# Performance work log

Measured on AMD Instinct MI355X. Metric: run time of the kernel, lower is better.

The kernel has to match this reference:

```python
import jax, jax.numpy as jnp
import numpy as np

RES = (128, 128, 128, 100)  # x, y, z, t resolutions
FEAT = 64
N = 1048576
HID = 64
COMBOS4 = [(0, 1), (0, 2), (0, 3), (1, 2), (1, 3), (2, 3)]  # temporal k-planes
COMBOS3 = [(0, 1), (0, 2), (1, 2)]  # spatial triplane


def setup_inputs() -> dict:
    key = jax.random.key(0)
    ks = jax.random.split(key, 16)
    d = {}
    d["inp"] = jax.random.uniform(ks[0], (N, 4), dtype=jnp.float32)  # xyz in [0,1], t in [0,1]
    d["aabb"] = jnp.array([[0.0, 0.0, 0.0], [1.0, 1.0, 1.0]], dtype=jnp.float32)
    # plane coefs: [feat, res[b], res[a]] per combo (a,b), uniform(init_a, init_b)
    for i, (a, b) in enumerate(COMBOS4):
        d[f"tp{i}"] = jax.random.uniform(ks[1 + i], (FEAT, RES[b], RES[a]),
                                         minval=0.1, maxval=0.5, dtype=jnp.float32)
    for i, (a, b) in enumerate(COMBOS3):
        d[f"sp{i}"] = jax.random.uniform(ks[7 + i], (FEAT, RES[b], RES[a]),
                                         minval=0.1, maxval=0.5, dtype=jnp.float32)
    in_dim = 2 * FEAT  # temporal + spatial features concatenated
    d["w0"] = (jax.random.normal(ks[10], (in_dim, HID), dtype=jnp.float32) / np.sqrt(in_dim)).astype(jnp.float32)
    d["b0"] = jnp.zeros((HID,), dtype=jnp.float32)
    d["w1"] = (jax.random.normal(ks[11], (HID, 3), dtype=jnp.float32) / np.sqrt(HID)).astype(jnp.float32)
    d["b1"] = jnp.zeros((3,), dtype=jnp.float32)
    return d


def _sample_plane(plane, cx, cy):
    """Bilinear grid_sample, align_corners=True. plane: [F,H,W]; cx,cy: [N] in [-1,1]. Returns [N,F]."""
    F_, H, W = plane.shape
    x = (cx + 1.0) * 0.5 * (W - 1)
    y = (cy + 1.0) * 0.5 * (H - 1)
    x0 = jnp.clip(jnp.floor(x).astype(jnp.int32), 0, W - 2)
    y0 = jnp.clip(jnp.floor(y).astype(jnp.int32), 0, H - 2)
    wx = (x - x0)[:, None]
    wy = (y - y0)[:, None]
    p = jnp.transpose(plane, (1, 2, 0))  # [H,W,F]
    v00 = p[y0, x0]
    v01 = p[y0, x0 + 1]
    v10 = p[y0 + 1, x0]
    v11 = p[y0 + 1, x0 + 1]
    return (v00 * (1 - wx) + v01 * wx) * (1 - wy) + (v10 * (1 - wx) + v11 * wx) * wy


def reference(inp, aabb, tp0, tp1, tp2, tp3, tp4, tp5, sp0, sp1, sp2, w0, b0, w1, b1):
    # normalize positions to [-1,1]
    pos = (inp[:, :3] - aabb[0]) / (aabb[1] - aabb[0]) * 2.0 - 1.0
    t = inp[:, 3:] * 2.0 - 1.0
    c = jnp.concatenate([pos, t], axis=-1)  # [N,4]
    tps = [tp0, tp1, tp2, tp3, tp4, tp5]
    feat_t = sum(_sample_plane(tps[i], c[:, a], c[:, b]) for i, (a, b) in enumerate(COMBOS4))
    sps = [sp0, sp1, sp2]
    feat_s = sum(_sample_plane(sps[i], pos[:, a], pos[:, b]) for i, (a, b) in enumerate(COMBOS3))
    feat = jnp.concatenate([feat_t, feat_s], axis=-1)  # [N, 2*FEAT]
    h = jax.nn.relu(feat @ w0 + b0)
    return h @ w1 + b1  # [N, 3]
```

## Files before the change

kernel.cpp:

```cpp
#include <hip/hip_runtime.h>
#include <hip/hip_fp16.h>

#define DEVFN __device__ __forceinline__

#if defined(__has_builtin)
#  if __has_builtin(__builtin_amdgcn_fdot2)
#    define HAS_FDOT2 1
#  endif
#endif

typedef _Float16 h2v __attribute__((ext_vector_type(2)));

struct PlanePtrs { const float* p[9]; };

__constant__ const int g_H[9] = {128,128,100,128,100,100,128,128,128};
__constant__ const int g_A[9] = {0,0,0,1,1,2,0,0,1};
__constant__ const int g_B[9] = {1,2,3,2,3,3,1,2,2};
__constant__ const int g_PRE[10] = {0,16384,32768,45568,61952,74752,87552,103936,120320,136704};
__constant__ const int g_OFF4[9] = {0,131072,262144,364544,495616,598016,700416,831488,962560};

static const int    TOTAL_TEXELS = 136704;
static const size_t WS_PLANES    = 17498112ull;
static const size_t WS_W0H       = 16384ull;
static const int    NBINS        = 2048;
static const int    NHB          = 256;

__global__ __launch_bounds__(256) void k_transpose(PlanePtrs ptrs, __half* __restrict__ dst)
{
    int gid = blockIdx.x * 256 + threadIdx.x;

    int pl = 0;
    #pragma unroll
    for (int i = 1; i < 9; ++i) if (gid >= g_PRE[i]) pl = i;
    int tx   = gid - g_PRE[pl];
    int nTex = g_PRE[pl + 1] - g_PRE[pl];

    const float* src = ptrs.p[0];
    #pragma unroll
    for (int i = 1; i < 9; ++i) if (pl == i) src = ptrs.p[i];
    src += tx;

    uint4* __restrict__ out4 = reinterpret_cast<uint4*>(dst) + (size_t)gid * 8;
    #pragma unroll
    for (int j = 0; j < 8; ++j) {
        float f0 = src[(8*j+0)*nTex];
        float f1 = src[(8*j+1)*nTex];
        float f2 = src[(8*j+2)*nTex];
        float f3 = src[(8*j+3)*nTex];
        float f4 = src[(8*j+4)*nTex];
        float f5 = src[(8*j+5)*nTex];
        float f6 = src[(8*j+6)*nTex];
        float f7 = src[(8*j+7)*nTex];
        uint4 u;
        u.x = __builtin_bit_cast(unsigned int, __floats2half2_rn(f0, f1));
        u.y = __builtin_bit_cast(unsigned int, __floats2half2_rn(f2, f3));
        u.z = __builtin_bit_cast(unsigned int, __floats2half2_rn(f4, f5));
        u.w = __builtin_bit_cast(unsigned int, __floats2half2_rn(f6, f7));
        out4[j] = u;
    }
}

__global__ __launch_bounds__(256) void k_w0pack(const float* __restrict__ w0,
                                                unsigned int* __restrict__ w0h)
{
    int idx = blockIdx.x * 256 + threadIdx.x;
    int d = idx >> 6, j = idx & 63;
    float a = w0[(2 * d) * 64 + j];
    float b = w0[(2 * d + 1) * 64 + j];
    w0h[idx] = __builtin_bit_cast(unsigned int, __floats2half2_rn(a, b));
}

DEVFN int point_key(float4 in, float a0x, float a0y, float a0z,
                    float isx, float isy, float isz)
{
    float x = (in.x - a0x) * isx;
    float y = (in.y - a0y) * isy;
    float z = (in.z - a0z) * isz;
    int xc = min(7, max(0, (int)(x * 8.0f)));
    int yc = min(7, max(0, (int)(y * 8.0f)));
    int zc = min(7, max(0, (int)(z * 8.0f)));
    int tc = min(3, max(0, (int)(in.w * 4.0f)));
    return (((xc << 3) | yc) << 3 | zc) << 2 | tc;
}

__global__ __launch_bounds__(256) void k_hist2(const float4* __restrict__ inp,
                                               const float* __restrict__ aabb,
                                               int N, int chunk,
                                               int* __restrict__ blkhist)
{
    __shared__ int hc[NBINS];
    const int tid = threadIdx.x, blk = blockIdx.x;
    #pragma unroll
    for (int j = 0; j < NBINS / 256; ++j) hc[tid + j * 256] = 0;
    __syncthreads();

    float a0x = aabb[0], a0y = aabb[1], a0z = aabb[2];
    float isx = 1.0f / (aabb[3] - a0x), isy = 1.0f / (aabb[4] - a0y), isz = 1.0f / (aabb[5] - a0z);

    int end = min(N, (blk + 1) * chunk);
    for (int i = blk * chunk + tid; i < end; i += 256)
        atomicAdd(&hc[point_key(inp[i], a0x, a0y, a0z, isx, isy, isz)], 1);

    __syncthreads();
    #pragma unroll
    for (int j = 0; j < NBINS / 256; ++j)
        blkhist[blk * NBINS + tid + j * 256] = hc[tid + j * 256];
}

__global__ __launch_bounds__(256) void k_scanA(int* __restrict__ blkhist,
                                               int* __restrict__ bintotal)
{
    int bin = blockIdx.x * 256 + threadIdx.x;
    int run = 0;
    for (int b = 0; b < NHB; ++b) {
        int v = blkhist[b * NBINS + bin];
        blkhist[b * NBINS + bin] = run;
        run += v;
    }
    bintotal[bin] = run;
}

__global__ __launch_bounds__(256) void k_scanB(const int* __restrict__ bintotal,
                                               int* __restrict__ binstart)
{
    int t = threadIdx.x;
    int v[8]; int sum = 0;
    #pragma unroll
    for (int j = 0; j < 8; ++j) { v[j] = bintotal[t * 8 + j]; sum += v[j]; }

    int lane = t & 63, w = t >> 6;
    int x = sum;
    #pragma unroll
    for (int d = 1; d < 64; d <<= 1) {
        int y = __shfl_up(x, d);
        if (lane >= d) x += y;
    }
    __shared__ int wsum[4];
    if (lane == 63) wsum[w] = x;
    __syncthreads();
    int woff = 0;
    for (int i = 0; i < w; ++i) woff += wsum[i];
    int run = woff + x - sum;
    #pragma unroll
    for (int j = 0; j < 8; ++j) { binstart[t * 8 + j] = run; run += v[j]; }
}

__global__ __launch_bounds__(256) void k_fill2(const float4* __restrict__ inp,
                                               const float* __restrict__ aabb,
                                               int N, int chunk,
                                               const int* __restrict__ blkhist,
                                               const int* __restrict__ binstart,
                                               int* __restrict__ order)
{
    __shared__ int hc[NBINS];
    const int tid = threadIdx.x, blk = blockIdx.x;
    #pragma unroll
    for (int j = 0; j < NBINS / 256; ++j) hc[tid + j * 256] = 0;
    __syncthreads();

    float a0x = aabb[0], a0y = aabb[1], a0z = aabb[2];
    float isx = 1.0f / (aabb[3] - a0x), isy = 1.0f / (aabb[4] - a0y), isz = 1.0f / (aabb[5] - a0z);

    int end = min(N, (blk + 1) * chunk);
    for (int i = blk * chunk + tid; i < end; i += 256) {
        int key = point_key(inp[i], a0x, a0y, a0z, isx, isy, isz);
        int lr  = atomicAdd(&hc[key], 1);
        order[binstart[key] + blkhist[blk * NBINS + key] + lr] = i;
    }
}

DEVFN void corner4f(unsigned a, unsigned b, unsigned c, unsigned d,
                    __half2 w00, __half2 w01, __half2 w10, __half2 w11,
                    float& ax, float& ay)
{
    __half2 t = __hmul2(__builtin_bit_cast(__half2, a), w00);
    t = __hfma2(__builtin_bit_cast(__half2, b), w01, t);
    t = __hfma2(__builtin_bit_cast(__half2, c), w10, t);
    t = __hfma2(__builtin_bit_cast(__half2, d), w11, t);
    ax += __low2float(t);
    ay += __high2float(t);
}

__global__ __launch_bounds__(64) void k_main(
    const float4* __restrict__ inp,
    const float*  __restrict__ aabb,
    const __half* __restrict__ planes,
    const unsigned int* __restrict__ w0h,
    const int*    __restrict__ order,
    int           useOrder,
    const float*  __restrict__ w0,
    const float*  __restrict__ b0,
    const float*  __restrict__ w1,
    const float*  __restrict__ b1,
    float*        __restrict__ out)
{
    __shared__ unsigned int lds[64 * 65];

    const int tid = threadIdx.x;
    const int g   = tid >> 3;
    const int k   = tid & 7;

    const int nwg = gridDim.x;
    const int bid = blockIdx.x;
    const int wid = ((nwg & 7) == 0) ? ((bid & 7) * (nwg >> 3) + (bid >> 3)) : bid;
    const int base = wid * 64;

    const int myord = useOrder ? order[base + tid] : (base + tid);

    float a0x = aabb[0], a0y = aabb[1], a0z = aabb[2];
    float sx  = aabb[3] - a0x, sy = aabb[4] - a0y, sz = aabb[5] - a0z;

    float4 min_ = inp[myord];
    float c0 = (min_.x - a0x) / sx * 2.0f - 1.0f;
    float c1 = (min_.y - a0y) / sy * 2.0f - 1.0f;
    float c2 = (min_.z - a0z) / sz * 2.0f - 1.0f;
    float c3 = min_.w * 2.0f - 1.0f;

    const uint4* pbase = reinterpret_cast<const uint4*>(planes);

    #pragma unroll 1
    for (int q = 0; q < 8; ++q) {
        const int p = g * 8 + q;
        float cc[4];
        cc[0] = __shfl(c0, p);
        cc[1] = __shfl(c1, p);
        cc[2] = __shfl(c2, p);
        cc[3] = __shfl(c3, p);

        int     offv[9];
        __half2 Wv[9][4];
        #pragma unroll
        for (int pl = 0; pl < 9; ++pl) {
            const int W = 128;
            const int H = g_H[pl];
            float fx = (cc[g_A[pl]] + 1.0f) * 0.5f * (float)(W - 1);
            float fy = (cc[g_B[pl]] + 1.0f) * 0.5f * (float)(H - 1);
            int x0 = min(max((int)floorf(fx), 0), W - 2);
            int y0 = min(max((int)floorf(fy), 0), H - 2);
            float wx = fx - (float)x0;
            float wy = fy - (float)y0;
            float iwx = 1.0f - wx, iwy = 1.0f - wy;
            offv[pl]  = g_OFF4[pl] + ((y0 << 7) + x0) * 8 + k;
            Wv[pl][0] = __float2half2_rn(iwx * iwy);
            Wv[pl][1] = __float2half2_rn(wx  * iwy);
            Wv[pl][2] = __float2half2_rn(iwx * wy);
            Wv[pl][3] = __float2half2_rn(wx  * wy);
        }

        uint4 v00[4], v01[4], v10[4], v11[4];
        #pragma unroll
        for (int s = 0; s < 4; ++s) {
            const uint4* pb = pbase + offv[s];
            v00[s] = pb[0];
            v01[s] = pb[8];
            v10[s] = pb[1024];
            v11[s] = pb[1032];
        }

        float accT[8], accS[8];
        #pragma unroll
        for (int j = 0; j < 8; ++j) { accT[j] = 0.0f; accS[j] = 0.0f; }

        #pragma unroll
        for (int pl = 0; pl < 9; ++pl) {
            const int s = pl & 3;
            if (pl < 6) {
                corner4f(v00[s].x, v01[s].x, v10[s].x, v11[s].x,
                         Wv[pl][0], Wv[pl][1], Wv[pl][2], Wv[pl][3], accT[0], accT[1]);
                corner4f(v00[s].y, v01[s].y, v10[s].y, v11[s].y,
                         Wv[pl][0], Wv[pl][1], Wv[pl][2], Wv[pl][3], accT[2], accT[3]);
                corner4f(v00[s].z, v01[s].z, v10[s].z, v11[s].z,
                         Wv[pl][0], Wv[pl][1], Wv[pl][2], Wv[pl][3], accT[4], accT[5]);
                corner4f(v00[s].w, v01[s].w, v10[s].w, v11[s].w,
                         Wv[pl][0], Wv[pl][1], Wv[pl][2], Wv[pl][3], accT[6], accT[7]);
            } else {
                corner4f(v00[s].x, v01[s].x, v10[s].x, v11[s].x,
                         Wv[pl][0], Wv[pl][1], Wv[pl][2], Wv[pl][3], accS[0], accS[1]);
                corner4f(v00[s].y, v01[s].y, v10[s].y, v11[s].y,
                         Wv[pl][0], Wv[pl][1], Wv[pl][2], Wv[pl][3], accS[2], accS[3]);
                corner4f(v00[s].z, v01[s].z, v10[s].z, v11[s].z,
                         Wv[pl][0], Wv[pl][1], Wv[pl][2], Wv[pl][3], accS[4], accS[5]);
                corner4f(v00[s].w, v01[s].w, v10[s].w, v11[s].w,
                         Wv[pl][0], Wv[pl][1], Wv[pl][2], Wv[pl][3], accS[6], accS[7]);
            }
            if (pl + 4 < 9) {
                const uint4* pb = pbase + offv[pl + 4];
                v00[s] = pb[0];
                v01[s] = pb[8];
                v10[s] = pb[1024];
                v11[s] = pb[1032];
            }
        }

        #pragma unroll
        for (int j = 0; j < 4; ++j) {
            lds[p * 65 +      k * 4 + j] =
                __builtin_bit_cast(unsigned int, __floats2half2_rn(accT[2*j], accT[2*j+1]));
            lds[p * 65 + 32 + k * 4 + j] =
                __builtin_bit_cast(unsigned int, __floats2half2_rn(accS[2*j], accS[2*j+1]));
        }
    }

    __syncthreads();

    const unsigned int* lrow = &lds[tid * 65];
    float o0 = b1[0], o1 = b1[1], o2 = b1[2];

    #pragma unroll 1
    for (int jc = 0; jc < 64; jc += 16) {
        float h[16];
        #pragma unroll
        for (int jj = 0; jj < 16; ++jj) h[jj] = b0[jc + jj];

        #pragma unroll 4
        for (int d = 0; d < 64; ++d) {
            unsigned u = lrow[d];
#if defined(HAS_FDOT2)
            h2v fv = __builtin_bit_cast(h2v, u);
            const unsigned int* wr = w0h + d * 64 + jc;
            #pragma unroll
            for (int jj = 0; jj < 16; ++jj)
                h[jj] = __builtin_amdgcn_fdot2(fv, __builtin_bit_cast(h2v, wr[jj]),
                                               h[jj], false);
#else
            __half2 hv = __builtin_bit_cast(__half2, u);
            float f0 = __low2float(hv);
            float f1 = __high2float(hv);
            const float* wr = w0 + d * 128 + jc;
            #pragma unroll
            for (int jj = 0; jj < 16; ++jj) h[jj] = fmaf(f0, wr[jj], h[jj]);
            #pragma unroll
            for (int jj = 0; jj < 16; ++jj) h[jj] = fmaf(f1, wr[64 + jj], h[jj]);
#endif
        }

        #pragma unroll
        for (int jj = 0; jj < 16; ++jj) {
            float r = fmaxf(h[jj], 0.0f);
            const float* wq = w1 + (jc + jj) * 3;
            o0 = fmaf(r, wq[0], o0);
            o1 = fmaf(r, wq[1], o1);
            o2 = fmaf(r, wq[2], o2);
        }
    }

    long long oo = (long long)myord * 3;
    out[oo + 0] = o0;
    out[oo + 1] = o1;
    out[oo + 2] = o2;
}

__global__ __launch_bounds__(256) void k_fallback(
    const float4* __restrict__ inp, const float* __restrict__ aabb, PlanePtrs ptrs,
    const float* __restrict__ w0, const float* __restrict__ b0,
    const float* __restrict__ w1, const float* __restrict__ b1,
    float* __restrict__ out, int N, int start)
{
    int pidx = start + blockIdx.x * 256 + threadIdx.x;
    if (pidx >= N) return;
    float4 in = inp[pidx];
    float c[4];
    c[0] = (in.x - aabb[0]) / (aabb[3] - aabb[0]) * 2.0f - 1.0f;
    c[1] = (in.y - aabb[1]) / (aabb[4] - aabb[1]) * 2.0f - 1.0f;
    c[2] = (in.z - aabb[2]) / (aabb[5] - aabb[2]) * 2.0f - 1.0f;
    c[3] = in.w * 2.0f - 1.0f;

    float h[64];
    #pragma unroll
    for (int j = 0; j < 64; ++j) h[j] = b0[j];

    #pragma unroll
    for (int pl = 0; pl < 9; ++pl) {
        const int W = 128, H = g_H[pl];
        float fx = (c[g_A[pl]] + 1.0f) * 0.5f * (float)(W - 1);
        float fy = (c[g_B[pl]] + 1.0f) * 0.5f * (float)(H - 1);
        int x0 = min(max((int)floorf(fx), 0), W - 2);
        int y0 = min(max((int)floorf(fy), 0), H - 2);
        float wx = fx - (float)x0, wy = fy - (float)y0;
        const float* P = ptrs.p[pl];
        int off = y0 * 128 + x0;
        int HW = H * 128;
        int row = (pl < 6) ? 0 : 64;
        for (int f = 0; f < 64; ++f) {
            const float* qp = P + f * HW + off;
            float v = (qp[0] * (1.0f - wx) + qp[1] * wx) * (1.0f - wy)
                    + (qp[128] * (1.0f - wx) + qp[129] * wx) * wy;
            const float* wr = w0 + (row + f) * 64;
            #pragma unroll
            for (int j = 0; j < 64; ++j) h[j] = fmaf(v, wr[j], h[j]);
        }
    }
    float o0 = b1[0], o1 = b1[1], o2 = b1[2];
    #pragma unroll
    for (int j = 0; j < 64; ++j) {
        float r = fmaxf(h[j], 0.0f);
        o0 = fmaf(r, w1[j * 3 + 0], o0);
        o1 = fmaf(r, w1[j * 3 + 1], o1);
        o2 = fmaf(r, w1[j * 3 + 2], o2);
    }
    out[(long long)pidx * 3 + 0] = o0;
    out[(long long)pidx * 3 + 1] = o1;
    out[(long long)pidx * 3 + 2] = o2;
}

extern "C" void kernel_launch(void* const* d_in, const int* in_sizes, int n_in,
                              void* d_out, int out_size, void* d_ws, size_t ws_size,
                              hipStream_t stream)
{
    const float4* inp  = (const float4*)d_in[0];
    const float*  aabb = (const float*)d_in[1];
    PlanePtrs ptrs;
    for (int i = 0; i < 9; ++i) ptrs.p[i] = (const float*)d_in[2 + i];
    const float* w0 = (const float*)d_in[11];
    const float* b0 = (const float*)d_in[12];
    const float* w1 = (const float*)d_in[13];
    const float* b1 = (const float*)d_in[14];
    float* out = (float*)d_out;
    const int N = in_sizes[0] / 4;

    const size_t off_w0h   = WS_PLANES;
    const size_t ws_base   = WS_PLANES + WS_W0H;
    const size_t off_order = ws_base;
    const size_t off_bh    = off_order + 4ull * (size_t)N;
    const size_t off_bt    = off_bh + (size_t)NHB * NBINS * 4;
    const size_t off_bs    = off_bt + NBINS * 4;
    const size_t need_sort = off_bs + NBINS * 4;

    if (ws_size >= ws_base && (N % 64) == 0) {
        __half* planes = (__half*)d_ws;
        unsigned int* w0h = (unsigned int*)((char*)d_ws + off_w0h);
        k_transpose<<<TOTAL_TEXELS / 256, 256, 0, stream>>>(ptrs, planes);
        k_w0pack<<<16, 256, 0, stream>>>(w0, w0h);

        if (ws_size >= need_sort) {
            int* order    = (int*)((char*)d_ws + off_order);
            int* blkhist  = (int*)((char*)d_ws + off_bh);
            int* bintotal = (int*)((char*)d_ws + off_bt);
            int* binstart = (int*)((char*)d_ws + off_bs);
            int chunk = (((N + NHB - 1) / NHB) + 255) / 256 * 256;

            k_hist2<<<NHB, 256, 0, stream>>>(inp, aabb, N, chunk, blkhist);
            k_scanA<<<NBINS / 256, 256, 0, stream>>>(blkhist, bintotal);
            k_scanB<<<1, 256, 0, stream>>>(bintotal, binstart);
            k_fill2<<<NHB, 256, 0, stream>>>(inp, aabb, N, chunk, blkhist, binstart, order);
            k_main<<<N / 64, 64, 0, stream>>>(inp, aabb, planes, w0h, order, 1,
                                              w0, b0, w1, b1, out);
        } else {
            k_main<<<N / 64, 64, 0, stream>>>(inp, aabb, planes, w0h, (const int*)nullptr, 0,
                                              w0, b0, w1, b1, out);
        }
    } else {
        k_fallback<<<(N + 255) / 256, 256, 0, stream>>>(inp, aabb, ptrs, w0, b0, w1, b1, out, N, 0);
    }
}
```

Baseline: 348.9 us.

## Split each 64-point block across two wavefronts with LDS partial-sum reduction

k_main now launches 128 threads per block, and each wave handles 32 points. The plane-gather loop shrinks from 8 to 4 iterations per wave, and in the MLP each wave computes half of the hidden units for all 64 points. Partial output sums are then reduced through LDS and wave 0 writes the result. This halves the serial per-thread work and adds a barrier and a small LDS reduction; launch_bounds(128,4) may limit registers.

Result: slower. 687.5 us (+97.1%).

```diff
diff --git a/kernel.cpp b/kernel.cpp
--- a/kernel.cpp
+++ b/kernel.cpp
@@ -181,7 +181,7 @@
     ay += __high2float(t);
 }
 
-__global__ __launch_bounds__(64) void k_main(
+__global__ __launch_bounds__(128, 4) void k_main(
     const float4* __restrict__ inp,
     const float*  __restrict__ aabb,
     const __half* __restrict__ planes,
@@ -194,9 +194,11 @@
     const float*  __restrict__ b1,
     float*        __restrict__ out)
 {
-    __shared__ unsigned int lds[64 * 65];
+    __shared__ unsigned int lds[64 * 65 + 64 + 192];
 
     const int tid = threadIdx.x;
+    const int wv  = tid >> 6;
+    const int ln  = tid & 63;
     const int g   = tid >> 3;
     const int k   = tid & 7;
 
@@ -205,7 +207,12 @@
     const int wid = ((nwg & 7) == 0) ? ((bid & 7) * (nwg >> 3) + (bid >> 3)) : bid;
     const int base = wid * 64;
 
-    const int myord = useOrder ? order[base + tid] : (base + tid);
+    const int mypt  = wv * 32 + (ln & 31);
+    const int myord = useOrder ? order[base + mypt] : (base + mypt);
+
+    unsigned int* ldsOrd  = &lds[64 * 65];
+    unsigned int* part    = &lds[64 * 65 + 64];
+    if (ln < 32) ldsOrd[mypt] = (unsigned)myord;
 
     float a0x = aabb[0], a0y = aabb[1], a0z = aabb[2];
     float sx  = aabb[3] - a0x, sy = aabb[4] - a0y, sz = aabb[5] - a0z;
@@ -219,13 +226,14 @@
     const uint4* pbase = reinterpret_cast<const uint4*>(planes);
 
     #pragma unroll 1
-    for (int q = 0; q < 8; ++q) {
-        const int p = g * 8 + q;
+    for (int q = 0; q < 4; ++q) {
+        const int lp = (g & 7) * 4 + q;
+        const int p  = wv * 32 + lp;
         float cc[4];
-        cc[0] = __shfl(c0, p);
-        cc[1] = __shfl(c1, p);
-        cc[2] = __shfl(c2, p);
-        cc[3] = __shfl(c3, p);
+        cc[0] = __shfl(c0, lp);
+        cc[1] = __shfl(c1, lp);
+        cc[2] = __shfl(c2, lp);
+        cc[3] = __shfl(c3, lp);
 
         int     offv[9];
         __half2 Wv[9][4];
@@ -303,11 +311,12 @@
 
     __syncthreads();
 
-    const unsigned int* lrow = &lds[tid * 65];
-    float o0 = b1[0], o1 = b1[1], o2 = b1[2];
+    const unsigned int* lrow = &lds[ln * 65];
+    float o0 = 0.0f, o1 = 0.0f, o2 = 0.0f;
 
     #pragma unroll 1
-    for (int jc = 0; jc < 64; jc += 16) {
+    for (int jc2 = 0; jc2 < 2; ++jc2) {
+        const int jc = wv * 32 + jc2 * 16;
         float h[16];
         #pragma unroll
         for (int jj = 0; jj < 16; ++jj) h[jj] = b0[jc + jj];
@@ -344,10 +353,23 @@
         }
     }
 
-    long long oo = (long long)myord * 3;
-    out[oo + 0] = o0;
-    out[oo + 1] = o1;
-    out[oo + 2] = o2;
+    if (wv == 1) {
+        part[ln * 3 + 0] = __builtin_bit_cast(unsigned int, o0);
+        part[ln * 3 + 1] = __builtin_bit_cast(unsigned int, o1);
+        part[ln * 3 + 2] = __builtin_bit_cast(unsigned int, o2);
+    }
+
+    __syncthreads();
+
+    if (wv == 0) {
+        float r0 = o0 + b1[0] + __builtin_bit_cast(float, part[ln * 3 + 0]);
+        float r1 = o1 + b1[1] + __builtin_bit_cast(float, part[ln * 3 + 1]);
+        float r2 = o2 + b1[2] + __builtin_bit_cast(float, part[ln * 3 + 2]);
+        long long oo = (long long)(int)ldsOrd[ln] * 3;
+        out[oo + 0] = r0;
+        out[oo + 1] = r1;
+        out[oo + 2] = r2;
+    }
 }
 
 __global__ __launch_bounds__(256) void k_fallback(
@@ -443,11 +465,11 @@
             k_scanA<<<NBINS / 256, 256, 0, stream>>>(blkhist, bintotal);
             k_scanB<<<1, 256, 0, stream>>>(bintotal, binstart);
             k_fill2<<<NHB, 256, 0, stream>>>(inp, aabb, N, chunk, blkhist, binstart, order);
-            k_main<<<N / 64, 64, 0, stream>>>(inp, aabb, planes, w0h, order, 1,
-                                              w0, b0, w1, b1, out);
+            k_main<<<N / 64, 128, 0, stream>>>(inp, aabb, planes, w0h, order, 1,
+                                               w0, b0, w1, b1, out);
         } else {
-            k_main<<<N / 64, 64, 0, stream>>>(inp, aabb, planes, w0h, (const int*)nullptr, 0,
-                                              w0, b0, w1, b1, out);
+            k_main<<<N / 64, 128, 0, stream>>>(inp, aabb, planes, w0h, (const int*)nullptr, 0,
+                                               w0, b0, w1, b1, out);
         }
     } else {
         k_fallback<<<(N + 255) / 256, 256, 0, stream>>>(inp, aabb, ptrs, w0, b0, w1, b1, out, N, 0);
```
